# Performance work log

Hardware: AMD Instinct MI355X
Metric: run time of the kernel (lower is better)

The kernel has to match this reference:

```python
import jax, jax.numpy as jnp
import numpy as np

INPUT, HIDDEN = 8, 16

def setup_inputs() -> dict:
    key = jax.random.key(0)
    ks = jax.random.split(key, 7)
    s_ih = 1.0 / np.sqrt(HIDDEN)
    x = jax.random.normal(ks[0], (8192, 512, INPUT), dtype=jnp.float32)
    W_ih = jax.random.uniform(ks[1], (HIDDEN, INPUT), jnp.float32, -s_ih, s_ih)
    W_hh = jax.random.uniform(ks[2], (HIDDEN, HIDDEN), jnp.float32, -s_ih, s_ih)
    b_ih = jax.random.uniform(ks[3], (HIDDEN,), jnp.float32, -s_ih, s_ih)
    b_hh = jax.random.uniform(ks[4], (HIDDEN,), jnp.float32, -s_ih, s_ih)
    s_fc = 1.0 / np.sqrt(HIDDEN)
    fc_w = jax.random.uniform(ks[5], (1, HIDDEN), jnp.float32, -s_fc, s_fc)
    fc_b = jax.random.uniform(ks[6], (1,), jnp.float32, -s_fc, s_fc)
    return {"x": x, "W_ih": W_ih, "W_hh": W_hh, "b_ih": b_ih, "b_hh": b_hh, "fc_w": fc_w, "fc_b": fc_b}

def reference(x, W_ih, W_hh, b_ih, b_hh, fc_w, fc_b):
    B, T, _ = x.shape
    # Precompute input projection for all timesteps: [B, T, H]
    xp = jnp.einsum('bti,hi->bth', x, W_ih) + b_ih + b_hh
    h0 = jnp.zeros((B, HIDDEN), dtype=x.dtype)

    def step(h, xt):
        h_new = jnp.tanh(xt + h @ W_hh.T)
        return h_new, None

    h_last, _ = jax.lax.scan(step, h0, jnp.swapaxes(xp, 0, 1))
    return h_last @ fc_w.T + fc_b  # [B, 1]
```

## Files before the change

### kernel.cpp

```cpp
#include <hip/hip_runtime.h>


#define RNN_B   8192
#define RNN_T   512
#define RNN_IN  8
#define RNN_H   16
#define TC      32
#define NB      16
#define XSTRIDE 264

template<int R>
__device__ __forceinline__ float ror16(float v) {
    return __int_as_float(__builtin_amdgcn_update_dpp(
        0, __float_as_int(v), 0x120 + R, 0xF, 0xF, false));
}

__global__ __launch_bounds__(256, 2) void rnn_fused_kernel(
    const float* __restrict__ x,
    const float* __restrict__ W_ih,
    const float* __restrict__ W_hh,
    const float* __restrict__ b_ih,
    const float* __restrict__ b_hh,
    const float* __restrict__ fc_w,
    const float* __restrict__ fc_b,
    float* __restrict__ out)
{
    __shared__ float xs[NB * XSTRIDE];

    const int tid = (int)threadIdx.x;
    const int j   = tid & 15;
    const int g   = tid >> 4;
    const int b0  = (int)blockIdx.x * NB;
    const int b   = b0 + g;

    float wperm[RNN_H];
#pragma unroll
    for (int r = 0; r < RNN_H; ++r) {
        wperm[r] = W_hh[j * RNN_H + ((j - r) & 15)];
    }
    float wih[RNN_IN];
#pragma unroll
    for (int i = 0; i < RNN_IN; i += 4) {
        float4 w = *(const float4*)(W_ih + j * RNN_IN + i);
        wih[i] = w.x; wih[i+1] = w.y; wih[i+2] = w.z; wih[i+3] = w.w;
    }
    const float bias = b_ih[j] + b_hh[j];

    float h = 0.0f;

    for (int t0 = 0; t0 < RNN_T; t0 += TC) {
        __syncthreads();
#pragma unroll
        for (int p = 0; p < 4; ++p) {
            int idx = tid + p * 256;
            int row = idx >> 6;
            int off = idx & 63;
            float4 v = *(const float4*)(x + ((size_t)(b0 + row) * RNN_T + t0) * RNN_IN + off * 4);
            *(float4*)(xs + row * XSTRIDE + off * 4) = v;
        }
        __syncthreads();

#pragma unroll 8
        for (int tt = 0; tt < TC; ++tt) {
            const float* xp = xs + g * XSTRIDE + tt * RNN_IN;
            const float4 xa = *(const float4*)(xp);
            const float4 xb = *(const float4*)(xp + 4);

            float a0 = fmaf(wih[0], xa.x, bias);
            a0 = fmaf(wih[1], xa.y, a0);
            a0 = fmaf(wih[2], xa.z, a0);
            a0 = fmaf(wih[3], xa.w, a0);

            float a1 = wih[4] * xb.x;
            a1 = fmaf(wih[5], xb.y, a1);
            a1 = fmaf(wih[6], xb.z, a1);
            a1 = fmaf(wih[7], xb.w, a1);

            float a2 = wperm[0] * h;
            float a3 = wperm[1] * ror16<1>(h);
            a0 = fmaf(wperm[2],  ror16<2>(h),  a0);
            a1 = fmaf(wperm[3],  ror16<3>(h),  a1);
            a2 = fmaf(wperm[4],  ror16<4>(h),  a2);
            a3 = fmaf(wperm[5],  ror16<5>(h),  a3);
            a0 = fmaf(wperm[6],  ror16<6>(h),  a0);
            a1 = fmaf(wperm[7],  ror16<7>(h),  a1);
            a2 = fmaf(wperm[8],  ror16<8>(h),  a2);
            a3 = fmaf(wperm[9],  ror16<9>(h),  a3);
            a0 = fmaf(wperm[10], ror16<10>(h), a0);
            a1 = fmaf(wperm[11], ror16<11>(h), a1);
            a2 = fmaf(wperm[12], ror16<12>(h), a2);
            a3 = fmaf(wperm[13], ror16<13>(h), a3);
            a0 = fmaf(wperm[14], ror16<14>(h), a0);
            a1 = fmaf(wperm[15], ror16<15>(h), a1);

            const float s = (a0 + a1) + (a2 + a3);

            const float e = __expf(s + s);
            const float r = __builtin_amdgcn_rcpf(e + 1.0f);
            h = fmaf(-2.0f, r, 1.0f);
        }
    }

    float v = h * fc_w[j];
    v += __shfl_xor(v, 1);
    v += __shfl_xor(v, 2);
    v += __shfl_xor(v, 4);
    v += __shfl_xor(v, 8);
    if (j == 0) out[b] = v + fc_b[0];
}

extern "C" void kernel_launch(void* const* d_in, const int* in_sizes, int n_in,
                              void* d_out, int out_size, void* d_ws, size_t ws_size,
                              hipStream_t stream)
{
    const float* x    = (const float*)d_in[0];
    const float* W_ih = (const float*)d_in[1];
    const float* W_hh = (const float*)d_in[2];
    const float* b_ih = (const float*)d_in[3];
    const float* b_hh = (const float*)d_in[4];
    const float* fc_w = (const float*)d_in[5];
    const float* fc_b = (const float*)d_in[6];
    float* out = (float*)d_out;

    dim3 grid(RNN_B / NB);
    dim3 block(256);
    rnn_fused_kernel<<<grid, block, 0, stream>>>(x, W_ih, W_hh, b_ih, b_hh, fc_w, fc_b, out);
}
```

Baseline: 269.4 us.

## Use single-wave blocks with register prefetch of next x chunk, drop barriers

```diff
diff --git a/kernel.cpp b/kernel.cpp
--- a/kernel.cpp
+++ b/kernel.cpp
@@ -6,7 +6,7 @@
 #define RNN_IN  8
 #define RNN_H   16
 #define TC      32
-#define NB      16
+#define NB      4
 #define XSTRIDE 264
 
 template<int R>
@@ -15,7 +15,7 @@
         0, __float_as_int(v), 0x120 + R, 0xF, 0xF, false));
 }
 
-__global__ __launch_bounds__(256, 2) void rnn_fused_kernel(
+__global__ __launch_bounds__(64, 2) void rnn_fused_kernel(
     const float* __restrict__ x,
     const float* __restrict__ W_ih,
     const float* __restrict__ W_hh,
@@ -46,58 +46,81 @@
     }
     const float bias = b_ih[j] + b_hh[j];
 
+    float4 gx[NB];
+
+#pragma unroll
+    for (int p = 0; p < NB; ++p) {
+        gx[p] = *(const float4*)(x + ((size_t)(b0 + p) * RNN_T + 0) * RNN_IN + tid * 4);
+    }
+#pragma unroll
+    for (int p = 0; p < NB; ++p) {
+        *(float4*)(xs + p * XSTRIDE + tid * 4) = gx[p];
+    }
+
     float h = 0.0f;
 
     for (int t0 = 0; t0 < RNN_T; t0 += TC) {
-        __syncthreads();
+        const bool more = (t0 + TC) < RNN_T;
+        if (more) {
 #pragma unroll
-        for (int p = 0; p < 4; ++p) {
-            int idx = tid + p * 256;
-            int row = idx >> 6;
-            int off = idx & 63;
-            float4 v = *(const float4*)(x + ((size_t)(b0 + row) * RNN_T + t0) * RNN_IN + off * 4);
-            *(float4*)(xs + row * XSTRIDE + off * 4) = v;
+            for (int p = 0; p < NB; ++p) {
+                gx[p] = *(const float4*)(x + ((size_t)(b0 + p) * RNN_T + (t0 + TC)) * RNN_IN + tid * 4);
+            }
         }
-        __syncthreads();
 
-#pragma unroll 8
-        for (int tt = 0; tt < TC; ++tt) {
-            const float* xp = xs + g * XSTRIDE + tt * RNN_IN;
-            const float4 xa = *(const float4*)(xp);
-            const float4 xb = *(const float4*)(xp + 4);
+        for (int u = 0; u < TC; u += 8) {
+            float4 xr[16];
+#pragma unroll
+            for (int s2 = 0; s2 < 8; ++s2) {
+                const float* xp = xs + g * XSTRIDE + (u + s2) * RNN_IN;
+                xr[2*s2]   = *(const float4*)(xp);
+                xr[2*s2+1] = *(const float4*)(xp + 4);
+            }
+#pragma unroll
+            for (int s2 = 0; s2 < 8; ++s2) {
+                const float4 xa = xr[2*s2];
+                const float4 xb = xr[2*s2+1];
 
-            float a0 = fmaf(wih[0], xa.x, bias);
-            a0 = fmaf(wih[1], xa.y, a0);
-            a0 = fmaf(wih[2], xa.z, a0);
-            a0 = fmaf(wih[3], xa.w, a0);
+                float a0 = fmaf(xa.x, wih[0], bias);
+                a0 = fmaf(xa.y, wih[1], a0);
+                a0 = fmaf(xa.z, wih[2], a0);
+                a0 = fmaf(xa.w, wih[3], a0);
 
-            float a1 = wih[4] * xb.x;
-            a1 = fmaf(wih[5], xb.y, a1);
-            a1 = fmaf(wih[6], xb.z, a1);
-            a1 = fmaf(wih[7], xb.w, a1);
+                float a1 = xb.x * wih[4];
+                a1 = fmaf(xb.y, wih[5], a1);
+                a1 = fmaf(xb.z, wih[6], a1);
+                a1 = fmaf(xb.w, wih[7], a1);
 
-            float a2 = wperm[0] * h;
-            float a3 = wperm[1] * ror16<1>(h);
-            a0 = fmaf(wperm[2],  ror16<2>(h),  a0);
-            a1 = fmaf(wperm[3],  ror16<3>(h),  a1);
-            a2 = fmaf(wperm[4],  ror16<4>(h),  a2);
-            a3 = fmaf(wperm[5],  ror16<5>(h),  a3);
-            a0 = fmaf(wperm[6],  ror16<6>(h),  a0);
-            a1 = fmaf(wperm[7],  ror16<7>(h),  a1);
-            a2 = fmaf(wperm[8],  ror16<8>(h),  a2);
-            a3 = fmaf(wperm[9],  ror16<9>(h),  a3);
-            a0 = fmaf(wperm[10], ror16<10>(h), a0);
-            a1 = fmaf(wperm[11], ror16<11>(h), a1);
-            a2 = fmaf(wperm[12], ror16<12>(h), a2);
-            a3 = fmaf(wperm[13], ror16<13>(h), a3);
-            a0 = fmaf(wperm[14], ror16<14>(h), a0);
-            a1 = fmaf(wperm[15], ror16<15>(h), a1);
+                float a2 = h * wperm[0];
+                float a3 = ror16<1>(h) * wperm[1];
+                a0 = fmaf(ror16<2>(h),  wperm[2],  a0);
+                a1 = fmaf(ror16<3>(h),  wperm[3],  a1);
+                a2 = fmaf(ror16<4>(h),  wperm[4],  a2);
+                a3 = fmaf(ror16<5>(h),  wperm[5],  a3);
+                a0 = fmaf(ror16<6>(h),  wperm[6],  a0);
+                a1 = fmaf(ror16<7>(h),  wperm[7],  a1);
+                a2 = fmaf(ror16<8>(h),  wperm[8],  a2);
+                a3 = fmaf(ror16<9>(h),  wperm[9],  a3);
+                a0 = fmaf(ror16<10>(h), wperm[10], a0);
+                a1 = fmaf(ror16<11>(h), wperm[11], a1);
+                a2 = fmaf(ror16<12>(h), wperm[12], a2);
+                a3 = fmaf(ror16<13>(h), wperm[13], a3);
+                a0 = fmaf(ror16<14>(h), wperm[14], a0);
+                a1 = fmaf(ror16<15>(h), wperm[15], a1);
 
-            const float s = (a0 + a1) + (a2 + a3);
+                const float s = (a0 + a1) + (a2 + a3);
 
-            const float e = __expf(s + s);
-            const float r = __builtin_amdgcn_rcpf(e + 1.0f);
-            h = fmaf(-2.0f, r, 1.0f);
+                const float e = __expf(s + s);
+                const float r = __builtin_amdgcn_rcpf(e + 1.0f);
+                h = fmaf(-2.0f, r, 1.0f);
+            }
+        }
+
+        if (more) {
+#pragma unroll
+            for (int p = 0; p < NB; ++p) {
+                *(float4*)(xs + p * XSTRIDE + tid * 4) = gx[p];
+            }
         }
     }
 
@@ -123,6 +146,6 @@
     float* out = (float*)d_out;
 
     dim3 grid(RNN_B / NB);
-    dim3 block(256);
+    dim3 block(64);
     rnn_fused_kernel<<<grid, block, 0, stream>>>(x, W_ih, W_hh, b_ih, b_hh, fc_w, fc_b, out);
 }
```

Result: slower. 292.0 us (+8.4%).

## Split each hidden-unit dot product across two lane halves with register prefetch

Applied to the files above, without the earlier changes.

```diff
diff --git a/kernel.cpp b/kernel.cpp
--- a/kernel.cpp
+++ b/kernel.cpp
@@ -6,8 +6,8 @@
 #define RNN_IN  8
 #define RNN_H   16
 #define TC      32
-#define NB      16
-#define XSTRIDE 264
+#define ROWS    8
+#define XST     264
 
 template<int R>
 __device__ __forceinline__ float ror16(float v) {
@@ -15,7 +15,7 @@
         0, __float_as_int(v), 0x120 + R, 0xF, 0xF, false));
 }
 
-__global__ __launch_bounds__(256, 2) void rnn_fused_kernel(
+__global__ __launch_bounds__(256, 4) void rnn_fused_kernel(
     const float* __restrict__ x,
     const float* __restrict__ W_ih,
     const float* __restrict__ W_hh,
@@ -25,79 +25,99 @@
     const float* __restrict__ fc_b,
     float* __restrict__ out)
 {
-    __shared__ float xs[NB * XSTRIDE];
+    __shared__ float xs[ROWS * XST];
 
-    const int tid = (int)threadIdx.x;
-    const int j   = tid & 15;
-    const int g   = tid >> 4;
-    const int b0  = (int)blockIdx.x * NB;
-    const int b   = b0 + g;
+    const int tid  = (int)threadIdx.x;
+    const int lane = tid & 63;
+    const int wv   = tid >> 6;
+    const int j    = lane & 15;
+    const int q    = (lane >> 4) & 1;
+    const int gb   = lane >> 5;
+    const int row  = 2 * wv + gb;
+    const int b0   = (int)blockIdx.x * ROWS;
+    const int b    = b0 + row;
 
-    float wperm[RNN_H];
+    const int oE = q ? (j ^ 8) : j;
+    const int oO = j;
+    float wrE[8], wrO[8];
 #pragma unroll
-    for (int r = 0; r < RNN_H; ++r) {
-        wperm[r] = W_hh[j * RNN_H + ((j - r) & 15)];
+    for (int r8 = 0; r8 < 8; ++r8) {
+        const int col = (j - r8) & 15;
+        wrE[r8] = W_hh[oE * RNN_H + col];
+        wrO[r8] = W_hh[oO * RNN_H + (q ? (col ^ 8) : col)];
     }
-    float wih[RNN_IN];
+    float wiE[4], wiO[4];
 #pragma unroll
-    for (int i = 0; i < RNN_IN; i += 4) {
-        float4 w = *(const float4*)(W_ih + j * RNN_IN + i);
-        wih[i] = w.x; wih[i+1] = w.y; wih[i+2] = w.z; wih[i+3] = w.w;
+    for (int i = 0; i < 4; ++i) {
+        wiE[i] = W_ih[oE * RNN_IN + q * 4 + i];
+        wiO[i] = W_ih[oO * RNN_IN + q * 4 + i];
     }
-    const float bias = b_ih[j] + b_hh[j];
+    const float biasE = q ? 0.0f : (b_ih[oE] + b_hh[oE]);
+    const float biasO = q ? 0.0f : (b_ih[oO] + b_hh[oO]);
+
+    const int r0 = tid >> 6,        f0 = tid & 63;
+    const int r1 = (tid + 256) >> 6;
+    const size_t goff0 = ((size_t)(b0 + r0) * RNN_T) * RNN_IN + f0 * 4;
+    const size_t goff1 = ((size_t)(b0 + r1) * RNN_T) * RNN_IN + f0 * 4;
+    float* const lws0 = xs + r0 * XST + f0 * 4;
+    float* const lws1 = xs + r1 * XST + f0 * 4;
+
+    float4 g0 = *(const float4*)(x + goff0);
+    float4 g1 = *(const float4*)(x + goff1);
+    *(float4*)lws0 = g0;
+    *(float4*)lws1 = g1;
+
+    const float* const xbase = xs + row * XST + q * 4;
+    const float KTANH = 2.8853900817779268f;
 
     float h = 0.0f;
 
     for (int t0 = 0; t0 < RNN_T; t0 += TC) {
         __syncthreads();
+        const bool more = (t0 + TC) < RNN_T;
+        if (more) {
+            g0 = *(const float4*)(x + goff0 + (size_t)(t0 + TC) * RNN_IN);
+            g1 = *(const float4*)(x + goff1 + (size_t)(t0 + TC) * RNN_IN);
+        }
+
+        float4 xr = *(const float4*)(xbase);
 #pragma unroll
-        for (int p = 0; p < 4; ++p) {
-            int idx = tid + p * 256;
-            int row = idx >> 6;
-            int off = idx & 63;
-            float4 v = *(const float4*)(x + ((size_t)(b0 + row) * RNN_T + t0) * RNN_IN + off * 4);
-            *(float4*)(xs + row * XSTRIDE + off * 4) = v;
+        for (int tt = 0; tt < TC; ++tt) {
+            const float4 xn = (tt + 1 < TC) ? *(const float4*)(xbase + (tt + 1) * RNN_IN) : xr;
+            const bool even = ((tt & 1) == 0);
+
+            const float* wr = even ? wrE : wrO;
+            const float* wi = even ? wiE : wiO;
+            const float bias = even ? biasE : biasO;
+
+            float c0 = fmaf(xr.x, wi[0], bias);
+            c0 = fmaf(xr.y, wi[1], c0);
+            c0 = fmaf(xr.z, wi[2], c0);
+            c0 = fmaf(xr.w, wi[3], c0);
+
+            float c1 = h * wr[0];
+            float c2 = ror16<1>(h) * wr[1];
+            c1 = fmaf(ror16<2>(h), wr[2], c1);
+            c2 = fmaf(ror16<3>(h), wr[3], c2);
+            c1 = fmaf(ror16<4>(h), wr[4], c1);
+            c2 = fmaf(ror16<5>(h), wr[5], c2);
+            c1 = fmaf(ror16<6>(h), wr[6], c1);
+            c2 = fmaf(ror16<7>(h), wr[7], c2);
+
+            const float sp = (c0 + c1) + c2;
+            const float s = sp + (even ? __shfl_xor(sp, 24) : __shfl_xor(sp, 16));
+
+            const float e  = __builtin_amdgcn_exp2f(s * KTANH);
+            const float rc = __builtin_amdgcn_rcpf(e + 1.0f);
+            h = fmaf(-2.0f, rc, 1.0f);
+
+            xr = xn;
         }
-        __syncthreads();
 
-#pragma unroll 8
-        for (int tt = 0; tt < TC; ++tt) {
-            const float* xp = xs + g * XSTRIDE + tt * RNN_IN;
-            const float4 xa = *(const float4*)(xp);
-            const float4 xb = *(const float4*)(xp + 4);
-
-            float a0 = fmaf(wih[0], xa.x, bias);
-            a0 = fmaf(wih[1], xa.y, a0);
-            a0 = fmaf(wih[2], xa.z, a0);
-            a0 = fmaf(wih[3], xa.w, a0);
-
-            float a1 = wih[4] * xb.x;
-            a1 = fmaf(wih[5], xb.y, a1);
-            a1 = fmaf(wih[6], xb.z, a1);
-            a1 = fmaf(wih[7], xb.w, a1);
-
-            float a2 = wperm[0] * h;
-            float a3 = wperm[1] * ror16<1>(h);
-            a0 = fmaf(wperm[2],  ror16<2>(h),  a0);
-            a1 = fmaf(wperm[3],  ror16<3>(h),  a1);
-            a2 = fmaf(wperm[4],  ror16<4>(h),  a2);
-            a3 = fmaf(wperm[5],  ror16<5>(h),  a3);
-            a0 = fmaf(wperm[6],  ror16<6>(h),  a0);
-            a1 = fmaf(wperm[7],  ror16<7>(h),  a1);
-            a2 = fmaf(wperm[8],  ror16<8>(h),  a2);
-            a3 = fmaf(wperm[9],  ror16<9>(h),  a3);
-            a0 = fmaf(wperm[10], ror16<10>(h), a0);
-            a1 = fmaf(wperm[11], ror16<11>(h), a1);
-            a2 = fmaf(wperm[12], ror16<12>(h), a2);
-            a3 = fmaf(wperm[13], ror16<13>(h), a3);
-            a0 = fmaf(wperm[14], ror16<14>(h), a0);
-            a1 = fmaf(wperm[15], ror16<15>(h), a1);
-
-            const float s = (a0 + a1) + (a2 + a3);
-
-            const float e = __expf(s + s);
-            const float r = __builtin_amdgcn_rcpf(e + 1.0f);
-            h = fmaf(-2.0f, r, 1.0f);
+        if (more) {
+            __syncthreads();
+            *(float4*)lws0 = g0;
+            *(float4*)lws1 = g1;
         }
     }
 
@@ -106,7 +126,7 @@
     v += __shfl_xor(v, 2);
     v += __shfl_xor(v, 4);
     v += __shfl_xor(v, 8);
-    if (j == 0) out[b] = v + fc_b[0];
+    if ((lane & 31) == 0) out[b] = v + fc_b[0];
 }
 
 extern "C" void kernel_launch(void* const* d_in, const int* in_sizes, int n_in,
@@ -122,7 +142,7 @@
     const float* fc_b = (const float*)d_in[6];
     float* out = (float*)d_out;
 
-    dim3 grid(RNN_B / NB);
+    dim3 grid(RNN_B / ROWS);
     dim3 block(256);
     rnn_fused_kernel<<<grid, block, 0, stream>>>(x, W_ih, W_hh, b_ih, b_hh, fc_w, fc_b, out);
 }
```

New measurement: 274.0 us. About the same (+1.7%).
